# Kernel tuning notes

Hardware: AMD Instinct MI355X
Metric: run time of the kernel (lower is better)

## Reference

```python
import jax, jax.numpy as jnp
import numpy as np

N_NODES = 50000
N_EDGES = 800000
D_FEAT = 64
IN_DIM = 1 + 2 * D_FEAT  # 129
FC_DIMS = [128, 64, 1]


def setup_inputs() -> dict:
    key = jax.random.key(0)
    ks = jax.random.split(key, 10)
    x = jax.random.normal(ks[0], (N_NODES, D_FEAT), dtype=jnp.float32)
    edge_index = jax.random.randint(ks[1], (2, N_EDGES), 0, N_NODES, dtype=jnp.int64)
    edge_weight = jax.random.uniform(ks[2], (N_EDGES, 1), dtype=jnp.float32)
    # MLP params (Linear: y = x @ W.T + b), Kaiming-ish scale
    dims = [IN_DIM] + FC_DIMS
    W1 = jax.random.normal(ks[3], (dims[1], dims[0]), dtype=jnp.float32) / np.sqrt(dims[0])
    b1 = jnp.zeros((dims[1],), dtype=jnp.float32)
    W2 = jax.random.normal(ks[4], (dims[2], dims[1]), dtype=jnp.float32) / np.sqrt(dims[1])
    b2 = jnp.zeros((dims[2],), dtype=jnp.float32)
    W3 = jax.random.normal(ks[5], (dims[3], dims[2]), dtype=jnp.float32) / np.sqrt(dims[2])
    b3 = jnp.zeros((dims[3],), dtype=jnp.float32)
    return {"x": x, "edge_index": edge_index, "edge_weight": edge_weight,
            "W1": W1, "b1": b1, "W2": W2, "b2": b2, "W3": W3, "b3": b3}


def reference(x, edge_index, edge_weight, W1, b1, W2, b2, W3, b3):
    # Gather source/target node features per edge: [E, d]
    src = x[edge_index[0]]
    tgt = x[edge_index[1]]
    # Concat [edge_weight | src | tgt] -> [E, 1 + 2d]
    h = jnp.concatenate([edge_weight, src, tgt], axis=1)
    # MLP (dropout is None / eval; last layer dim==1 -> no ReLU)
    h = jax.nn.relu(h @ W1.T + b1)
    h = jax.nn.relu(h @ W2.T + b2)
    return h @ W3.T + b3  # [E, 1] new edge weights
```

## Files before the change

kernel.cpp:

```cpp
#include <hip/hip_runtime.h>

typedef _Float16 half8 __attribute__((ext_vector_type(8)));
typedef _Float16 half4_t __attribute__((ext_vector_type(4)));
typedef float floatx4 __attribute__((ext_vector_type(4)));

__device__ __forceinline__ int swz(int row, int col) {
    return row * 128 + (col ^ ((row & 7) << 3));
}

__global__ __launch_bounds__(256) void prep_kernel(
    const float* __restrict__ x,
    const float* __restrict__ W1, const float* __restrict__ W2,
    const float* __restrict__ b1, const float* __restrict__ b2,
    const float* __restrict__ W3,
    _Float16* __restrict__ wsh, float* __restrict__ pf,
    _Float16* __restrict__ xh, int n_x8)
{
    int b = blockIdx.x;
    if (b < 96) {
        int tid = b * 256 + threadIdx.x;
        if (tid < 16384) {
            int c = tid >> 9, r = tid & 511;
            int L = r >> 3, jj = r & 7;
            int mt = c >> 2, kb = c & 3;
            int n = mt * 16 + (L & 15);
            int k = kb * 32 + (L >> 4) * 8 + jj;
            wsh[tid] = (_Float16)W1[n * 129 + 1 + k];
        } else {
            int t = tid - 16384;
            int c = t >> 9, r = t & 511;
            int L = r >> 3, jj = r & 7;
            int it = c >> 2, kb = c & 3;
            int i = it * 16 + (L & 15);
            int j = kb * 32 + (L >> 4) * 8 + jj;
            wsh[tid] = (_Float16)W2[i * 128 + j];
        }
    } else if (b == 96) {
        for (int i = threadIdx.x; i < 384; i += 256) {
            float v;
            if (i < 128)      v = b1[i];
            else if (i < 256) v = W1[(i - 128) * 129];
            else if (i < 320) v = b2[i - 256];
            else              v = W3[i - 320];
            pf[i] = v;
        }
    } else {
        int t2 = (b - 97) * 256 + threadIdx.x;
        if (t2 < n_x8) {
            const float4* p = (const float4*)(x + (size_t)t2 * 8);
            float4 v0 = p[0], v1 = p[1];
            half8 h = {(_Float16)v0.x, (_Float16)v0.y, (_Float16)v0.z, (_Float16)v0.w,
                       (_Float16)v1.x, (_Float16)v1.y, (_Float16)v1.z, (_Float16)v1.w};
            *(half8*)(xh + (size_t)t2 * 8) = h;
        }
    }
}

__global__ __launch_bounds__(256, 4) void edge_mlp_kernel(
    const _Float16* __restrict__ xh,
    const int* __restrict__ ei,
    const float* __restrict__ ew,
    const float* __restrict__ b3,
    const _Float16* __restrict__ wf,
    const float* __restrict__ pf,
    float* __restrict__ out, int E)
{
    __shared__ __align__(16) _Float16 hA[64 * 128];
    __shared__ float s_out[4][64];

    const int tid  = threadIdx.x;
    const int lane = tid & 63;
    const int wave = tid >> 6;
    const int lrow = lane & 15;
    const int quad = lane >> 4;
    const int e_blk = blockIdx.x * 64;

    {
        int e_loc = tid & 63;
        int part = (tid >> 6) & 1;
        int half = tid >> 7;
        int e = e_blk + e_loc; if (e >= E) e = E - 1;
        int node = ei[(size_t)part * E + e];
        const _Float16* rp = xh + (size_t)node * 64 + half * 32;
        int r7 = (e_loc & 7) << 3;
        _Float16* dst = &hA[e_loc * 128];
        int base = part * 64 + half * 32;
#pragma unroll
        for (int q = 0; q < 4; ++q)
            *(half8*)(dst + ((base + q * 8) ^ r7)) = *(const half8*)(rp + q * 8);
    }

    float ewv[4];
#pragma unroll
    for (int nt = 0; nt < 4; ++nt) {
        int e = e_blk + nt * 16 + lrow; if (e >= E) e = E - 1;
        ewv[nt] = ew[e];
    }
    const float b3v = b3[0];

    __syncthreads();

    half4_t h1v[2][4];
#pragma unroll
    for (int mi = 0; mi < 2; ++mi) {
        const int mt = 2 * wave + mi;
        half8 afr[4];
#pragma unroll
        for (int kb = 0; kb < 4; ++kb)
            afr[kb] = *(const half8*)(wf + (mt * 4 + kb) * 512 + lane * 8);
        int nb = mt * 16 + quad * 4;
        float4 b1v = *(const float4*)(pf + nb);
        float4 c0v = *(const float4*)(pf + 128 + nb);
#pragma unroll
        for (int nt = 0; nt < 4; ++nt) {
            int row = nt * 16 + lrow;
            half8 bfr[4];
#pragma unroll
            for (int kb = 0; kb < 4; ++kb)
                bfr[kb] = *(const half8*)(&hA[swz(row, kb * 32 + quad * 8)]);
            floatx4 a = {0.f, 0.f, 0.f, 0.f};
#pragma unroll
            for (int kb = 0; kb < 4; ++kb)
                a = __builtin_amdgcn_mfma_f32_16x16x32_f16(afr[kb], bfr[kb], a, 0, 0, 0);
            half4_t hv;
            hv[0] = (_Float16)fmaxf(a[0] + b1v.x + ewv[nt] * c0v.x, 0.f);
            hv[1] = (_Float16)fmaxf(a[1] + b1v.y + ewv[nt] * c0v.y, 0.f);
            hv[2] = (_Float16)fmaxf(a[2] + b1v.z + ewv[nt] * c0v.z, 0.f);
            hv[3] = (_Float16)fmaxf(a[3] + b1v.w + ewv[nt] * c0v.w, 0.f);
            h1v[mi][nt] = hv;
        }
    }
    __syncthreads();

#pragma unroll
    for (int mi = 0; mi < 2; ++mi) {
        int nb = (2 * wave + mi) * 16 + quad * 4;
#pragma unroll
        for (int nt = 0; nt < 4; ++nt)
            *(half4_t*)(&hA[swz(nt * 16 + lrow, nb)]) = h1v[mi][nt];
    }
    __syncthreads();

    half8 a2[4];
#pragma unroll
    for (int kb = 0; kb < 4; ++kb)
        a2[kb] = *(const half8*)(wf + 16384 + (wave * 4 + kb) * 512 + lane * 8);
    int ib = wave * 16 + quad * 4;
    float4 b2v = *(const float4*)(pf + 256 + ib);
    float4 w3v = *(const float4*)(pf + 320 + ib);

#pragma unroll
    for (int nt = 0; nt < 4; ++nt) {
        int row = nt * 16 + lrow;
        half8 bfr[4];
#pragma unroll
        for (int kb = 0; kb < 4; ++kb)
            bfr[kb] = *(const half8*)(&hA[swz(row, kb * 32 + quad * 8)]);
        floatx4 a = {0.f, 0.f, 0.f, 0.f};
#pragma unroll
        for (int kb = 0; kb < 4; ++kb)
            a = __builtin_amdgcn_mfma_f32_16x16x32_f16(a2[kb], bfr[kb], a, 0, 0, 0);
        float p = fmaxf(a[0] + b2v.x, 0.f) * w3v.x;
        p      += fmaxf(a[1] + b2v.y, 0.f) * w3v.y;
        p      += fmaxf(a[2] + b2v.z, 0.f) * w3v.z;
        p      += fmaxf(a[3] + b2v.w, 0.f) * w3v.w;
        p += __shfl_xor(p, 16, 64);
        p += __shfl_xor(p, 32, 64);
        if (quad == 0) s_out[wave][nt * 16 + lrow] = p;
    }
    __syncthreads();

    if (tid < 64) {
        int oe = e_blk + tid;
        if (oe < E)
            out[oe] = b3v + s_out[0][tid] + s_out[1][tid]
                          + s_out[2][tid] + s_out[3][tid];
    }
}

extern "C" void kernel_launch(void* const* d_in, const int* in_sizes, int n_in,
                              void* d_out, int out_size, void* d_ws, size_t ws_size,
                              hipStream_t stream) {
    const float* x  = (const float*)d_in[0];
    const int*   ei = (const int*)d_in[1];
    const float* ew = (const float*)d_in[2];
    const float* W1 = (const float*)d_in[3];
    const float* b1 = (const float*)d_in[4];
    const float* W2 = (const float*)d_in[5];
    const float* b2 = (const float*)d_in[6];
    const float* W3 = (const float*)d_in[7];
    const float* b3 = (const float*)d_in[8];
    float* out = (float*)d_out;
    const int E = in_sizes[2];
    const int n_x = in_sizes[0];
    const int n_x8 = n_x / 8;

    _Float16* wsh = (_Float16*)d_ws;
    float*    pf  = (float*)((char*)d_ws + 49152);
    _Float16* xh  = (_Float16*)((char*)d_ws + 51200);

    int xblk = (n_x8 + 255) / 256;
    prep_kernel<<<97 + xblk, 256, 0, stream>>>(x, W1, W2, b1, b2, W3,
                                               wsh, pf, xh, n_x8);

    int nblk = (E + 63) / 64;
    edge_mlp_kernel<<<nblk, 256, 0, stream>>>(xh, ei, ew, b3, wsh, pf, out, E);
}
```

Before: 142.8 us.

## Gather node rows directly into LDS and repartition layer-2 work per wave

Node-feature gathering now goes straight from global memory into shared memory through global_load_lds, with lane addresses chosen to land in the same XOR-swizzled layout, so the data no longer passes through registers. The layer-1 weight fragments are hoisted and loaded before the barrier, and the loop order is switched so each B fragment is read from LDS once for both M tiles. Layer 2 is repartitioned so each wave owns 16 edges across all 64 outputs, which removes the cross-wave s_out reduction and its barrier. In exchange, each wave now loads all of W2 instead of a quarter of it, and correctness depends on the async LDS writes being complete when the barrier is reached.

```diff
diff --git a/kernel.cpp b/kernel.cpp
--- a/kernel.cpp
+++ b/kernel.cpp
@@ -66,7 +66,6 @@
     float* __restrict__ out, int E)
 {
     __shared__ __align__(16) _Float16 hA[64 * 128];
-    __shared__ float s_out[4][64];
 
     const int tid  = threadIdx.x;
     const int lane = tid & 63;
@@ -75,19 +74,18 @@
     const int quad = lane >> 4;
     const int e_blk = blockIdx.x * 64;
 
-    {
-        int e_loc = tid & 63;
-        int part = (tid >> 6) & 1;
-        int half = tid >> 7;
-        int e = e_blk + e_loc; if (e >= E) e = E - 1;
+#pragma unroll
+    for (int i = 0; i < 4; ++i) {
+        int row = wave * 16 + i * 4 + quad;
+        int c = lrow ^ (row & 7);
+        int part = c >> 3;
+        int e = e_blk + row; if (e >= E) e = E - 1;
         int node = ei[(size_t)part * E + e];
-        const _Float16* rp = xh + (size_t)node * 64 + half * 32;
-        int r7 = (e_loc & 7) << 3;
-        _Float16* dst = &hA[e_loc * 128];
-        int base = part * 64 + half * 32;
-#pragma unroll
-        for (int q = 0; q < 4; ++q)
-            *(half8*)(dst + ((base + q * 8) ^ r7)) = *(const half8*)(rp + q * 8);
+        const _Float16* g = xh + (size_t)node * 64 + (c & 7) * 8;
+        __builtin_amdgcn_global_load_lds(
+            (const __attribute__((address_space(1))) void*)g,
+            (__attribute__((address_space(3))) void*)&hA[wave * 2048 + i * 512],
+            16, 0, 0);
     }
 
     float ewv[4];
@@ -98,30 +96,32 @@
     }
     const float b3v = b3[0];
 
+    half8 afr[2][4];
+#pragma unroll
+    for (int mi = 0; mi < 2; ++mi)
+#pragma unroll
+        for (int kb = 0; kb < 4; ++kb)
+            afr[mi][kb] = *(const half8*)(wf + ((2 * wave + mi) * 4 + kb) * 512 + lane * 8);
+
     __syncthreads();
 
     half4_t h1v[2][4];
 #pragma unroll
-    for (int mi = 0; mi < 2; ++mi) {
-        const int mt = 2 * wave + mi;
-        half8 afr[4];
-#pragma unroll
-        for (int kb = 0; kb < 4; ++kb)
-            afr[kb] = *(const half8*)(wf + (mt * 4 + kb) * 512 + lane * 8);
-        int nb = mt * 16 + quad * 4;
-        float4 b1v = *(const float4*)(pf + nb);
-        float4 c0v = *(const float4*)(pf + 128 + nb);
-#pragma unroll
-        for (int nt = 0; nt < 4; ++nt) {
-            int row = nt * 16 + lrow;
-            half8 bfr[4];
+    for (int nt = 0; nt < 4; ++nt) {
+        int row = nt * 16 + lrow;
+        half8 bfr[4];
+#pragma unroll
+        for (int kb = 0; kb < 4; ++kb)
+            bfr[kb] = *(const half8*)(&hA[swz(row, kb * 32 + quad * 8)]);
+#pragma unroll
+        for (int mi = 0; mi < 2; ++mi) {
+            floatx4 a = {0.f, 0.f, 0.f, 0.f};
 #pragma unroll
             for (int kb = 0; kb < 4; ++kb)
-                bfr[kb] = *(const half8*)(&hA[swz(row, kb * 32 + quad * 8)]);
-            floatx4 a = {0.f, 0.f, 0.f, 0.f};
-#pragma unroll
-            for (int kb = 0; kb < 4; ++kb)
-                a = __builtin_amdgcn_mfma_f32_16x16x32_f16(afr[kb], bfr[kb], a, 0, 0, 0);
+                a = __builtin_amdgcn_mfma_f32_16x16x32_f16(afr[mi][kb], bfr[kb], a, 0, 0, 0);
+            int nb = (2 * wave + mi) * 16 + quad * 4;
+            float4 b1v = *(const float4*)(pf + nb);
+            float4 c0v = *(const float4*)(pf + 128 + nb);
             half4_t hv;
             hv[0] = (_Float16)fmaxf(a[0] + b1v.x + ewv[nt] * c0v.x, 0.f);
             hv[1] = (_Float16)fmaxf(a[1] + b1v.y + ewv[nt] * c0v.y, 0.f);
@@ -141,40 +141,38 @@
     }
     __syncthreads();
 
-    half8 a2[4];
+    const int erow = wave * 16 + lrow;
+    half8 b2fr[4];
 #pragma unroll
     for (int kb = 0; kb < 4; ++kb)
-        a2[kb] = *(const half8*)(wf + 16384 + (wave * 4 + kb) * 512 + lane * 8);
-    int ib = wave * 16 + quad * 4;
-    float4 b2v = *(const float4*)(pf + 256 + ib);
-    float4 w3v = *(const float4*)(pf + 320 + ib);
-
-#pragma unroll
-    for (int nt = 0; nt < 4; ++nt) {
-        int row = nt * 16 + lrow;
-        half8 bfr[4];
-#pragma unroll
-        for (int kb = 0; kb < 4; ++kb)
-            bfr[kb] = *(const half8*)(&hA[swz(row, kb * 32 + quad * 8)]);
+        b2fr[kb] = *(const half8*)(&hA[swz(erow, kb * 32 + quad * 8)]);
+
+    float tot = b3v;
+#pragma unroll
+    for (int it = 0; it < 4; ++it) {
+        half8 a2[4];
+#pragma unroll
+        for (int kb = 0; kb < 4; ++kb)
+            a2[kb] = *(const half8*)(wf + 16384 + (it * 4 + kb) * 512 + lane * 8);
+        int ib = it * 16 + quad * 4;
+        float4 b2v = *(const float4*)(pf + 256 + ib);
+        float4 w3v = *(const float4*)(pf + 320 + ib);
         floatx4 a = {0.f, 0.f, 0.f, 0.f};
 #pragma unroll
         for (int kb = 0; kb < 4; ++kb)
-            a = __builtin_amdgcn_mfma_f32_16x16x32_f16(a2[kb], bfr[kb], a, 0, 0, 0);
+            a = __builtin_amdgcn_mfma_f32_16x16x32_f16(a2[kb], b2fr[kb], a, 0, 0, 0);
         float p = fmaxf(a[0] + b2v.x, 0.f) * w3v.x;
         p      += fmaxf(a[1] + b2v.y, 0.f) * w3v.y;
         p      += fmaxf(a[2] + b2v.z, 0.f) * w3v.z;
         p      += fmaxf(a[3] + b2v.w, 0.f) * w3v.w;
         p += __shfl_xor(p, 16, 64);
         p += __shfl_xor(p, 32, 64);
-        if (quad == 0) s_out[wave][nt * 16 + lrow] = p;
-    }
-    __syncthreads();
-
-    if (tid < 64) {
-        int oe = e_blk + tid;
-        if (oe < E)
-            out[oe] = b3v + s_out[0][tid] + s_out[1][tid]
-                          + s_out[2][tid] + s_out[3][tid];
+        tot += p;
+    }
+
+    if (quad == 0) {
+        int oe = e_blk + erow;
+        if (oe < E) out[oe] = tot;
     }
 }
 
```

Measured after the change: 149.9 us. 5.0% more time.
